# Optimization experiments

Measured on AMD Instinct MI355X. Metric: run time of the kernel, lower is better.

The kernel has to match this reference:

```python
import jax, jax.numpy as jnp
import numpy as np

NEG_SLOPE = 0.2  # PyG GATConv default negative_slope
EPS = 1e-16      # PyG softmax denominator epsilon


def gat_conv(x, W, att_src, att_dst, bias, src, dst, num_nodes, concat):
    H, C = att_src.shape
    h = (x @ W).reshape(-1, H, C)                    # [N,H,C]
    a_src = jnp.einsum('nhc,hc->nh', h, att_src)      # [N,H]
    a_dst = jnp.einsum('nhc,hc->nh', h, att_dst)      # [N,H]
    e = a_src[src] + a_dst[dst]                       # [E,H]
    e = jax.nn.leaky_relu(e, NEG_SLOPE)
    # segment softmax over incoming edges of each destination node
    e_max = jax.ops.segment_max(e, dst, num_segments=num_nodes)   # [N,H]
    e_max = jnp.where(jnp.isfinite(e_max), e_max, 0.0)
    p = jnp.exp(e - e_max[dst])                        # [E,H]
    denom = jax.ops.segment_sum(p, dst, num_segments=num_nodes)   # [N,H]
    alpha = p / (denom[dst] + EPS)                     # [E,H]
    msg = h[src] * alpha[:, :, None]                   # [E,H,C]
    out = jax.ops.segment_sum(msg, dst, num_segments=num_nodes)   # [N,H,C]
    if concat:
        out = out.reshape(num_nodes, H * C)
    else:
        out = out.mean(axis=1)
    return out + bias


def setup_inputs() -> dict:
    key = jax.random.key(0)
    ks = jax.random.split(key, 10)
    N, E, Fin, H, C, OUT = 50000, 400000, 128, 8, 32, 32
    s = 0.05
    return {
        'x': jax.random.normal(ks[0], (N, Fin), jnp.float32),
        'edge_index': jax.random.randint(ks[1], (2, E), 0, N, jnp.int64),
        'W1': jax.random.normal(ks[2], (Fin, H * C), jnp.float32) * s,
        'att_src1': jax.random.normal(ks[3], (H, C), jnp.float32) * s,
        'att_dst1': jax.random.normal(ks[4], (H, C), jnp.float32) * s,
        'b1': jax.random.normal(ks[5], (H * C,), jnp.float32) * s,
        'W2': jax.random.normal(ks[6], (H * C, H * OUT), jnp.float32) * s,
        'att_src2': jax.random.normal(ks[7], (H, OUT), jnp.float32) * s,
        'att_dst2': jax.random.normal(ks[8], (H, OUT), jnp.float32) * s,
        'b2': jax.random.normal(ks[9], (OUT,), jnp.float32) * s,
    }


def reference(x, edge_index, W1, att_src1, att_dst1, b1, W2, att_src2, att_dst2, b2):
    N = x.shape[0]
    src, dst = edge_index[0], edge_index[1]
    h = gat_conv(x, W1, att_src1, att_dst1, b1, src, dst, N, concat=True)
    h = jax.nn.elu(h)  # dropout p=0 / eval: identity
    out = gat_conv(h, W2, att_src2, att_dst2, b2, src, dst, N, concat=False)
    return out
```

## Files before the change

kernel.cpp:

```cpp
#include <hip/hip_runtime.h>
#include <math.h>

#define NEG_SLOPE 0.2f

typedef float f32x4 __attribute__((ext_vector_type(4)));
typedef short bf16x8 __attribute__((ext_vector_type(8)));
typedef unsigned short ushortv8 __attribute__((ext_vector_type(8)));

__device__ __forceinline__ unsigned short f2bf(float f) {
    union { float f; unsigned u; } uu; uu.f = f;
    unsigned r = uu.u + 0x7FFF + ((uu.u >> 16) & 1);
    return (unsigned short)(r >> 16);
}
__device__ __forceinline__ float bf2f(unsigned short u) {
    union { unsigned u; float f; } x; x.u = ((unsigned)u) << 16; return x.f;
}

__global__ void prep_kernel(const float* __restrict__ W1, unsigned short* __restrict__ Wt1,
                            const float* __restrict__ W2, unsigned short* __restrict__ Wt2,
                            int* __restrict__ counts, int* __restrict__ cursor, int N)
{
    int u = blockIdx.x * 256 + threadIdx.x;
    if (u < 32768) {
        int nn = u >> 7, k = u & 127;
        Wt1[u] = f2bf(W1[(size_t)k * 256 + nn]);
        return;
    }
    u -= 32768;
    if (u < 65536) {
        int nn = u >> 8, k = u & 255;
        Wt2[u] = f2bf(W2[(size_t)k * 256 + nn]);
        return;
    }
    u -= 65536;
    if (u < N) { counts[u] = 0; cursor[u] = 0; }
}

__global__ void hist_kernel(const int* __restrict__ dst, int* __restrict__ counts, int E)
{
    int e = blockIdx.x * 256 + threadIdx.x;
    if (e < E) atomicAdd(&counts[dst[e]], 1);
}

template<int CVT>
__global__ __launch_bounds__(256) void gemm_mfma(
    const void* __restrict__ Av,
    const unsigned short* __restrict__ Bt,
    unsigned short* __restrict__ C,
    const float* __restrict__ att_s,
    const float* __restrict__ att_d,
    float* __restrict__ a_s,
    float* __restrict__ a_d,
    int M, int K)
{
    __shared__ unsigned short As[128 * 64];
    __shared__ unsigned short Bs[128 * 64];
    const int tid  = threadIdx.x;
    const int lane = tid & 63;
    const int wave = tid >> 6;
    const int wr = wave >> 1, wc = wave & 1;
    const int row0 = blockIdx.y * 128;
    const int col0 = blockIdx.x * 128;

    f32x4 acc[4][4] = {};

    for (int k0 = 0; k0 < K; k0 += 64) {
        ushortv8 va[4], vb[4];
        #pragma unroll
        for (int i = 0; i < 4; ++i) {
            int c  = i * 256 + tid;
            int r  = c >> 3, cc = c & 7;
            int ga = row0 + r; if (ga >= M) ga = M - 1;
            if constexpr (CVT) {
                const float* ap = (const float*)Av + (size_t)ga * K + k0 + cc * 8;
                float4 lo = *(const float4*)ap;
                float4 hi = *(const float4*)(ap + 4);
                ushortv8 o;
                o[0]=f2bf(lo.x); o[1]=f2bf(lo.y); o[2]=f2bf(lo.z); o[3]=f2bf(lo.w);
                o[4]=f2bf(hi.x); o[5]=f2bf(hi.y); o[6]=f2bf(hi.z); o[7]=f2bf(hi.w);
                va[i] = o;
            } else {
                va[i] = *(const ushortv8*)((const unsigned short*)Av +
                                           (size_t)ga * K + k0 + cc * 8);
            }
            vb[i] = *(const ushortv8*)(Bt + (size_t)(col0 + r) * K + k0 + cc * 8);
        }
        __syncthreads();
        #pragma unroll
        for (int i = 0; i < 4; ++i) {
            int c  = i * 256 + tid;
            int r  = c >> 3, cc = c & 7;
            int sl = cc ^ (r & 7);
            *(ushortv8*)(As + r * 64 + sl * 8) = va[i];
            *(ushortv8*)(Bs + r * 64 + sl * 8) = vb[i];
        }
        __syncthreads();

        #pragma unroll
        for (int kk = 0; kk < 2; ++kk) {
            const int kbyte = kk * 64 + ((lane >> 4) << 4);
            bf16x8 af[4], bfr[4];
            #pragma unroll
            for (int m = 0; m < 4; ++m) {
                int r = wr * 64 + m * 16 + (lane & 15);
                af[m] = *(const bf16x8*)((const char*)As + r * 128 + (kbyte ^ ((r & 7) << 4)));
            }
            #pragma unroll
            for (int n = 0; n < 4; ++n) {
                int r = wc * 64 + n * 16 + (lane & 15);
                bfr[n] = *(const bf16x8*)((const char*)Bs + r * 128 + (kbyte ^ ((r & 7) << 4)));
            }
            #pragma unroll
            for (int m = 0; m < 4; ++m)
                #pragma unroll
                for (int n = 0; n < 4; ++n)
                    acc[m][n] = __builtin_amdgcn_mfma_f32_16x16x32_bf16(
                        af[m], bfr[n], acc[m][n], 0, 0, 0);
        }
        __syncthreads();
    }

    #pragma unroll
    for (int m = 0; m < 4; ++m) {
        int rbase = row0 + wr * 64 + m * 16 + ((lane >> 4) << 2);
        #pragma unroll
        for (int j = 0; j < 4; ++j) {
            int grow = rbase + j;
            if (grow < M) {
                #pragma unroll
                for (int n = 0; n < 4; ++n)
                    C[(size_t)grow * 256 + col0 + wc * 64 + n * 16 + (lane & 15)] =
                        f2bf(acc[m][n][j]);
            }
        }
    }

    float asv[4], adv[4];
    #pragma unroll
    for (int n = 0; n < 4; ++n) {
        int colg = col0 + wc * 64 + n * 16 + (lane & 15);
        asv[n] = att_s[colg];
        adv[n] = att_d[colg];
    }
    const int hbase = blockIdx.x * 4 + wc * 2;
    #pragma unroll
    for (int m = 0; m < 4; ++m) {
        int rbase = row0 + wr * 64 + m * 16 + ((lane >> 4) << 2);
        #pragma unroll
        for (int j = 0; j < 4; ++j) {
            int grow = rbase + j;
            #pragma unroll
            for (int t = 0; t < 2; ++t) {
                float vs = acc[m][2*t][j] * asv[2*t] + acc[m][2*t+1][j] * asv[2*t+1];
                float vd = acc[m][2*t][j] * adv[2*t] + acc[m][2*t+1][j] * adv[2*t+1];
                #pragma unroll
                for (int off = 1; off < 16; off <<= 1) {
                    vs += __shfl_xor(vs, off);
                    vd += __shfl_xor(vd, off);
                }
                if ((lane & 15) == 0 && grow < M) {
                    a_s[(size_t)grow * 8 + hbase + t] = vs;
                    a_d[(size_t)grow * 8 + hbase + t] = vd;
                }
            }
        }
    }
}

__global__ __launch_bounds__(256) void scan_blk(
    const int* __restrict__ counts, int* __restrict__ incl, int* __restrict__ bsum, int N)
{
    __shared__ int wtot[4], wexc[4];
    int t = blockIdx.x * 256 + threadIdx.x;
    int lane = threadIdx.x & 63, wid = threadIdx.x >> 6;
    int v = (t < N) ? counts[t] : 0;
    int s = v;
    #pragma unroll
    for (int off = 1; off < 64; off <<= 1) {
        int u = __shfl_up(s, off);
        if (lane >= off) s += u;
    }
    if (lane == 63) wtot[wid] = s;
    __syncthreads();
    if (threadIdx.x == 0) {
        int r = 0;
        #pragma unroll
        for (int w = 0; w < 4; ++w) { wexc[w] = r; r += wtot[w]; }
    }
    __syncthreads();
    int out = s + wexc[wid];
    if (t < N) incl[t] = out;
    if (threadIdx.x == 255) bsum[blockIdx.x] = out;
}

__global__ __launch_bounds__(256) void scan_top(int* __restrict__ bsum, int nb)
{
    __shared__ int wtot[4], wexc[4];
    int tid = threadIdx.x;
    int lane = tid & 63, wid = tid >> 6;
    int v = (tid < nb) ? bsum[tid] : 0;
    int s = v;
    #pragma unroll
    for (int off = 1; off < 64; off <<= 1) {
        int u = __shfl_up(s, off);
        if (lane >= off) s += u;
    }
    if (lane == 63) wtot[wid] = s;
    __syncthreads();
    if (tid == 0) {
        int r = 0;
        #pragma unroll
        for (int w = 0; w < 4; ++w) { wexc[w] = r; r += wtot[w]; }
    }
    __syncthreads();
    if (tid < nb) bsum[tid] = s + wexc[wid] - v;
}

__global__ void fill_kernel(const int* __restrict__ src, const int* __restrict__ dst,
                            const int* __restrict__ incl, const int* __restrict__ bsum,
                            int* __restrict__ rowptr, int* __restrict__ cursor,
                            int* __restrict__ esrc, int N, int E)
{
    int t = blockIdx.x * 256 + threadIdx.x;
    if (t < N) {
        rowptr[t + 1] = incl[t] + bsum[t >> 8];
        if (t == 0) rowptr[0] = 0;
    }
    if (t < E) {
        int d = dst[t];
        int rp = bsum[d >> 8] + ((d & 255) ? incl[d - 1] : 0);
        int pos = rp + atomicAdd(&cursor[d], 1);
        esrc[pos] = src[t];
    }
}

template<int LAYER>
__global__ __launch_bounds__(128) void gat_agg(
    const unsigned short* __restrict__ h, const float* __restrict__ a_s,
    const float* __restrict__ a_d, const int* __restrict__ rowptr,
    const int* __restrict__ esrc, const float* __restrict__ bias,
    float* __restrict__ out, unsigned short* __restrict__ out_b, int N)
{
    const int n  = blockIdx.x * 4 + (threadIdx.x >> 5);
    if (n >= N) return;
    const int sl   = threadIdx.x & 31;
    const int head = sl >> 2;
    const int beg = rowptr[n];
    const int deg = rowptr[n + 1] - beg;

    const float adn = a_d[(size_t)n*8 + head];
    float dsum = 0.f;
    float2 acc2[4] = {{0.f,0.f},{0.f,0.f},{0.f,0.f},{0.f,0.f}};

    int j0 = 0;
    for (; j0 + 4 <= deg; j0 += 4) {
        int s0 = esrc[beg + j0 + 0];
        int s1 = esrc[beg + j0 + 1];
        int s2 = esrc[beg + j0 + 2];
        int s3 = esrc[beg + j0 + 3];
        int sv[4] = {s0, s1, s2, s3};
        #pragma unroll
        for (int k = 0; k < 4; ++k) {
            int s = sv[k];
            float e = a_s[(size_t)s*8 + head] + adn;
            e = fmaxf(e, NEG_SLOPE * e);
            float p = __expf(e);
            dsum += p;
            uint4 hv = *(const uint4*)(h + (size_t)s*256 + sl*8);
            const unsigned* hw = (const unsigned*)&hv;
            #pragma unroll
            for (int i = 0; i < 4; ++i) {
                acc2[i].x += p * __uint_as_float(hw[i] << 16);
                acc2[i].y += p * __uint_as_float(hw[i] & 0xffff0000u);
            }
        }
    }
    for (; j0 < deg; ++j0) {
        int s = esrc[beg + j0];
        float e = a_s[(size_t)s*8 + head] + adn;
        e = fmaxf(e, NEG_SLOPE * e);
        float p = __expf(e);
        dsum += p;
        uint4 hv = *(const uint4*)(h + (size_t)s*256 + sl*8);
        const unsigned* hw = (const unsigned*)&hv;
        #pragma unroll
        for (int i = 0; i < 4; ++i) {
            acc2[i].x += p * __uint_as_float(hw[i] << 16);
            acc2[i].y += p * __uint_as_float(hw[i] & 0xffff0000u);
        }
    }

    float invd = 1.f / (dsum + 1e-16f);

    if (LAYER == 1) {
        ushortv8 o;
        #pragma unroll
        for (int i = 0; i < 4; ++i) {
            float v0 = acc2[i].x * invd + bias[sl*8 + 2*i];
            float v1 = acc2[i].y * invd + bias[sl*8 + 2*i + 1];
            o[2*i]   = f2bf(v0 > 0.f ? v0 : expf(v0) - 1.f);
            o[2*i+1] = f2bf(v1 > 0.f ? v1 : expf(v1) - 1.f);
        }
        *(ushortv8*)(out_b + (size_t)n*256 + sl*8) = o;
    } else {
        #pragma unroll
        for (int i = 0; i < 4; ++i) { acc2[i].x *= invd; acc2[i].y *= invd; }
        #pragma unroll
        for (int m = 4; m <= 16; m <<= 1)
            #pragma unroll
            for (int i = 0; i < 4; ++i) {
                acc2[i].x += __shfl_xor(acc2[i].x, m);
                acc2[i].y += __shfl_xor(acc2[i].y, m);
            }
        if (sl < 4) {
            float4 lo = make_float4(acc2[0].x*0.125f + bias[sl*8+0],
                                    acc2[0].y*0.125f + bias[sl*8+1],
                                    acc2[1].x*0.125f + bias[sl*8+2],
                                    acc2[1].y*0.125f + bias[sl*8+3]);
            float4 hi = make_float4(acc2[2].x*0.125f + bias[sl*8+4],
                                    acc2[2].y*0.125f + bias[sl*8+5],
                                    acc2[3].x*0.125f + bias[sl*8+6],
                                    acc2[3].y*0.125f + bias[sl*8+7]);
            *(float4*)(out + (size_t)n*32 + sl*8)     = lo;
            *(float4*)(out + (size_t)n*32 + sl*8 + 4) = hi;
        }
    }
}

extern "C" void kernel_launch(void* const* d_in, const int* in_sizes, int n_in,
                              void* d_out, int out_size, void* d_ws, size_t ws_size,
                              hipStream_t stream)
{
    const float* x   = (const float*)d_in[0];
    const int*   ei  = (const int*)  d_in[1];
    const float* W1  = (const float*)d_in[2];
    const float* as1 = (const float*)d_in[3];
    const float* ad1 = (const float*)d_in[4];
    const float* b1  = (const float*)d_in[5];
    const float* W2  = (const float*)d_in[6];
    const float* as2 = (const float*)d_in[7];
    const float* ad2 = (const float*)d_in[8];
    const float* b2  = (const float*)d_in[9];

    const int N = in_sizes[0] / 128;
    const int E = in_sizes[1] / 2;
    const int* srcp = ei;
    const int* dstp = ei + E;

    char* ws = (char*)d_ws;
    unsigned short* hb    = (unsigned short*)ws;  ws += (size_t)N * 256 * 2;
    unsigned short* out1b = (unsigned short*)ws;  ws += (size_t)N * 256 * 2;
    unsigned short* Wt1   = (unsigned short*)ws;  ws += 256 * 128 * 2;
    unsigned short* Wt2   = (unsigned short*)ws;  ws += 256 * 256 * 2;
    float*          a_s   = (float*)ws;           ws += (size_t)N * 8 * 4;
    float*          a_d   = (float*)ws;           ws += (size_t)N * 8 * 4;
    int*            counts= (int*)ws;             ws += (size_t)N * 4;
    int*            cursor= (int*)ws;             ws += (size_t)N * 4;
    int*            incl  = (int*)ws;             ws += (size_t)N * 4;
    int*            bsum  = (int*)ws;             ws += 256 * 4;
    int*            rowptr= (int*)ws;             ws += (size_t)(N + 1) * 4;
    int*            esrc  = (int*)ws;

    const int nb = (N + 255) / 256;

    {
        int tot = 32768 + 65536 + N;
        prep_kernel<<<(tot + 255) / 256, 256, 0, stream>>>(
            W1, Wt1, W2, Wt2, counts, cursor, N);
    }
    hist_kernel<<<(E + 255) / 256, 256, 0, stream>>>(dstp, counts, E);
    scan_blk<<<nb, 256, 0, stream>>>(counts, incl, bsum, N);
    scan_top<<<1, 256, 0, stream>>>(bsum, nb);
    fill_kernel<<<(E + 255) / 256, 256, 0, stream>>>(srcp, dstp, incl, bsum,
                                                     rowptr, cursor, esrc, N, E);

    const int gridM = (N + 127) / 128;

    gemm_mfma<1><<<dim3(2, gridM), 256, 0, stream>>>(x, Wt1, hb, as1, ad1,
                                                     a_s, a_d, N, 128);
    gat_agg<1><<<(N + 3) / 4, 128, 0, stream>>>(hb, a_s, a_d, rowptr, esrc, b1,
                                                nullptr, out1b, N);

    gemm_mfma<0><<<dim3(2, gridM), 256, 0, stream>>>(out1b, Wt2, hb, as2, ad2,
                                                     a_s, a_d, N, 256);
    gat_agg<2><<<(N + 3) / 4, 128, 0, stream>>>(hb, a_s, a_d, rowptr, esrc, b2,
                                                (float*)d_out, nullptr, N);
}
```

Measured before the change: 186.9 us.

## Compute full 256-column output tile per block so A rows load once

```diff
diff --git a/kernel.cpp b/kernel.cpp
--- a/kernel.cpp
+++ b/kernel.cpp
@@ -43,7 +43,7 @@
 }
 
 template<int CVT>
-__global__ __launch_bounds__(256) void gemm_mfma(
+__global__ __launch_bounds__(512) void gemm_mfma(
     const void* __restrict__ Av,
     const unsigned short* __restrict__ Bt,
     unsigned short* __restrict__ C,
@@ -54,21 +54,20 @@
     int M, int K)
 {
     __shared__ unsigned short As[128 * 64];
-    __shared__ unsigned short Bs[128 * 64];
+    __shared__ unsigned short Bs[256 * 64];
     const int tid  = threadIdx.x;
     const int lane = tid & 63;
     const int wave = tid >> 6;
-    const int wr = wave >> 1, wc = wave & 1;
-    const int row0 = blockIdx.y * 128;
-    const int col0 = blockIdx.x * 128;
+    const int wr = wave >> 2, wc = wave & 3;
+    const int row0 = blockIdx.x * 128;
 
     f32x4 acc[4][4] = {};
 
     for (int k0 = 0; k0 < K; k0 += 64) {
-        ushortv8 va[4], vb[4];
-        #pragma unroll
-        for (int i = 0; i < 4; ++i) {
-            int c  = i * 256 + tid;
+        ushortv8 va[2], vb[4];
+        #pragma unroll
+        for (int i = 0; i < 2; ++i) {
+            int c  = i * 512 + tid;
             int r  = c >> 3, cc = c & 7;
             int ga = row0 + r; if (ga >= M) ga = M - 1;
             if constexpr (CVT) {
@@ -83,16 +82,25 @@
                 va[i] = *(const ushortv8*)((const unsigned short*)Av +
                                            (size_t)ga * K + k0 + cc * 8);
             }
-            vb[i] = *(const ushortv8*)(Bt + (size_t)(col0 + r) * K + k0 + cc * 8);
+        }
+        #pragma unroll
+        for (int i = 0; i < 4; ++i) {
+            int c  = i * 512 + tid;
+            int r  = c >> 3, cc = c & 7;
+            vb[i] = *(const ushortv8*)(Bt + (size_t)r * K + k0 + cc * 8);
         }
         __syncthreads();
         #pragma unroll
+        for (int i = 0; i < 2; ++i) {
+            int c  = i * 512 + tid;
+            int r  = c >> 3, cc = c & 7;
+            *(ushortv8*)(As + r * 64 + (cc ^ (r & 7)) * 8) = va[i];
+        }
+        #pragma unroll
         for (int i = 0; i < 4; ++i) {
-            int c  = i * 256 + tid;
+            int c  = i * 512 + tid;
             int r  = c >> 3, cc = c & 7;
-            int sl = cc ^ (r & 7);
-            *(ushortv8*)(As + r * 64 + sl * 8) = va[i];
-            *(ushortv8*)(Bs + r * 64 + sl * 8) = vb[i];
+            *(ushortv8*)(Bs + r * 64 + (cc ^ (r & 7)) * 8) = vb[i];
         }
         __syncthreads();
 
@@ -129,7 +137,7 @@
             if (grow < M) {
                 #pragma unroll
                 for (int n = 0; n < 4; ++n)
-                    C[(size_t)grow * 256 + col0 + wc * 64 + n * 16 + (lane & 15)] =
+                    C[(size_t)grow * 256 + wc * 64 + n * 16 + (lane & 15)] =
                         f2bf(acc[m][n][j]);
             }
         }
@@ -138,11 +146,11 @@
     float asv[4], adv[4];
     #pragma unroll
     for (int n = 0; n < 4; ++n) {
-        int colg = col0 + wc * 64 + n * 16 + (lane & 15);
+        int colg = wc * 64 + n * 16 + (lane & 15);
         asv[n] = att_s[colg];
         adv[n] = att_d[colg];
     }
-    const int hbase = blockIdx.x * 4 + wc * 2;
+    const int hbase = wc * 2;
     #pragma unroll
     for (int m = 0; m < 4; ++m) {
         int rbase = row0 + wr * 64 + m * 16 + ((lane >> 4) << 2);
@@ -376,13 +384,13 @@
 
     const int gridM = (N + 127) / 128;
 
-    gemm_mfma<1><<<dim3(2, gridM), 256, 0, stream>>>(x, Wt1, hb, as1, ad1,
-                                                     a_s, a_d, N, 128);
+    gemm_mfma<1><<<gridM, 512, 0, stream>>>(x, Wt1, hb, as1, ad1,
+                                            a_s, a_d, N, 128);
     gat_agg<1><<<(N + 3) / 4, 128, 0, stream>>>(hb, a_s, a_d, rowptr, esrc, b1,
                                                 nullptr, out1b, N);
 
-    gemm_mfma<0><<<dim3(2, gridM), 256, 0, stream>>>(out1b, Wt2, hb, as2, ad2,
-                                                     a_s, a_d, N, 256);
+    gemm_mfma<0><<<gridM, 512, 0, stream>>>(out1b, Wt2, hb, as2, ad2,
+                                            a_s, a_d, N, 256);
     gat_agg<2><<<(N + 3) / 4, 128, 0, stream>>>(hb, a_s, a_d, rowptr, esrc, b2,
                                                 (float*)d_out, nullptr, N);
 }
```

Measured after the change: 176.0 us. -5.8%, faster.
